# Optimization experiments

Hardware: AMD Instinct MI355X
Metric: run time of the kernel (lower is better)

## Reference

```python
import jax, jax.numpy as jnp
import numpy as np

D = 256  # model dim, used for 1/sqrt(d) scaling


def setup_inputs() -> dict:
    key = jax.random.key(0)
    ks = jax.random.split(key, 6)
    B, N, Dm, K = 4, 8192, 256, 256
    s = 0.02
    return {
        "I": jax.random.normal(ks[0], (B, N, Dm), dtype=jnp.float32),
        "Wq": jax.random.normal(ks[1], (Dm, Dm), dtype=jnp.float32) * s,
        "Wk": jax.random.normal(ks[2], (Dm, Dm), dtype=jnp.float32) * s,
        "Wv": jax.random.normal(ks[3], (Dm, Dm), dtype=jnp.float32) * s,
        "We": jax.random.normal(ks[4], (K, N), dtype=jnp.float32) * s,
        "Wf": jax.random.normal(ks[5], (K, N), dtype=jnp.float32) * s,
    }


def reference(I, Wq, Wk, Wv, We, Wf):
    # I: [B, n, d]; nn.Linear applies x @ W.T
    Q = jnp.einsum("bnd,ed->bne", I, Wq)          # [B, n, d]
    K = jnp.einsum("bnd,ed->bne", I, Wk)          # [B, n, d]
    V = jnp.einsum("bnd,ed->bne", I, Wv)          # [B, n, d]
    # E projects K along the sequence axis: K^T [B,d,n] -> [B,d,k]
    Ke = jnp.einsum("bnd,kn->bdk", K, We)         # [B, d, k]
    # F projects V along the sequence axis, then transpose back: [B,k,d]
    Vf = jnp.einsum("bnd,kn->bkd", V, Wf)         # [B, k, d]
    scale = 1.0 / jnp.sqrt(jnp.asarray(D, dtype=Q.dtype))
    PBar = jnp.einsum("bnd,bdk->bnk", Q, Ke) * scale  # [B, n, k]
    PBar = jax.nn.softmax(PBar, axis=2)
    # dropout omitted (eval / deterministic reference)
    Head = jnp.einsum("bnk,bkd->bnd", PBar, Vf)   # [B, n, d]
    return Head
```

## Files before the change

kernel.cpp:

```cpp
#include <hip/hip_runtime.h>
#include <stdint.h>


typedef unsigned short u16;
typedef __attribute__((ext_vector_type(8))) __bf16 bf16x8;
typedef __attribute__((ext_vector_type(4))) float f32x4;
typedef __attribute__((ext_vector_type(4))) unsigned short u16x4;
typedef __attribute__((ext_vector_type(8))) unsigned short u16x8;

__device__ __forceinline__ u16 f2bf(float f) {
  unsigned int u = __float_as_uint(f);
  u += 0x7FFFu + ((u >> 16) & 1u);
  return (u16)(u >> 16);
}

__device__ __forceinline__ void gld_lds16(const void* g, void* l) {
  __builtin_amdgcn_global_load_lds((const __attribute__((address_space(1))) void*)g,
                                   (__attribute__((address_space(3))) void*)l, 16, 0, 0);
}

__device__ __forceinline__ void stage_tile(const u16* src, long long ld, long long kb,
                                           u16* lds, int tid) {
#pragma unroll
  for (int r = 0; r < 4; ++r) {
    const int off = r * 4096 + tid * 16;
    const int row = off >> 7;
    const int colb = (off & 127) ^ ((row & 7) << 4);
    gld_lds16(src + (long long)row * ld + kb + (colb >> 1), (char*)lds + off);
  }
}

__device__ __forceinline__ void mfma_step(const u16* Alds, const u16* Blds, int lane, int wr,
                                          int wc, f32x4 (&acc)[4][4]) {
#pragma unroll
  for (int kk = 0; kk < 2; ++kk) {
    const int ko2 = (kk * 32 + (lane >> 4) * 8) * 2;
    bf16x8 a[4], b[4];
#pragma unroll
    for (int m = 0; m < 4; ++m) {
      const int ar = wr + m * 16 + (lane & 15);
      a[m] = *(const bf16x8*)((const char*)Alds + ((ar * 128 + ko2) ^ ((ar & 7) << 4)));
    }
#pragma unroll
    for (int n = 0; n < 4; ++n) {
      const int br = wc + n * 16 + (lane & 15);
      b[n] = *(const bf16x8*)((const char*)Blds + ((br * 128 + ko2) ^ ((br & 7) << 4)));
    }
#pragma unroll
    for (int m = 0; m < 4; ++m)
#pragma unroll
      for (int n = 0; n < 4; ++n)
        acc[m][n] = __builtin_amdgcn_mfma_f32_16x16x32_bf16(a[m], b[n], acc[m][n], 0, 0, 0);
  }
}

__global__ __launch_bounds__(256) void k0(const float* __restrict__ I,
                                          const float* __restrict__ Wq,
                                          const float* __restrict__ Wk,
                                          const float* __restrict__ Wv,
                                          const float* __restrict__ We,
                                          const float* __restrict__ Wf,
                                          u16* __restrict__ Ibf, u16* __restrict__ IT,
                                          u16* __restrict__ WqT, u16* __restrict__ WkT,
                                          u16* __restrict__ WvB, u16* __restrict__ WeB,
                                          u16* __restrict__ WfB) {
  const int p = blockIdx.x, t = threadIdx.x;
  if (p < 2080) {
    __shared__ u16 T[4096];
    const float* src;
    u16 *dT, *dS;
    long long srow, scol, tld;
    if (p < 2048) {
      const int b = p >> 9, id = p & 511;
      src = I + (long long)b * 2097152;
      srow = (long long)(id >> 2) * 64;
      scol = (long long)(id & 3) * 64;
      dS = Ibf + (long long)b * 2097152;
      dT = IT + (long long)b * 2097152;
      tld = 8192;
    } else {
      const int q = p - 2048;
      src = (q < 16) ? Wq : Wk;
      const int id = q & 15;
      srow = (long long)(id >> 2) * 64;
      scol = (long long)(id & 3) * 64;
      dS = nullptr;
      dT = (q < 16) ? WqT : WkT;
      tld = 256;
    }
    const int cc = t & 15, rL = t >> 4;
#pragma unroll
    for (int i = 0; i < 4; ++i) {
      const int r = rL + 16 * i;
      f32x4 v = *(const f32x4*)(src + (srow + r) * 256 + scol + cc * 4);
      u16x4 o = {f2bf(v[0]), f2bf(v[1]), f2bf(v[2]), f2bf(v[3])};
      if (dS) *(u16x4*)(dS + (srow + r) * 256 + scol + cc * 4) = o;
      const int P = (cc + (r & 15) + 4 * (r >> 4)) & 15;
      *(u16x4*)&T[r * 64 + P * 4] = o;
    }
    __syncthreads();
    const int dd = t >> 2, ch2 = t & 3;
    u16 buf[16];
#pragma unroll
    for (int j = 0; j < 16; ++j) {
      const int P = ((dd >> 2) + j + 4 * ch2) & 15;
      buf[j] = T[(ch2 * 16 + j) * 64 + P * 4 + (dd & 3)];
    }
    u16* dp = dT + (scol + dd) * tld + srow + ch2 * 16;
    *(u16x8*)dp = *(u16x8*)&buf[0];
    *(u16x8*)(dp + 8) = *(u16x8*)&buf[8];
  } else {
    const long long base = (long long)(p - 2080) * 4096;
#pragma unroll
    for (int rnd = 0; rnd < 4; ++rnd) {
      const long long e = base + rnd * 1024 + t * 4;
      const float* s;
      u16* d;
      long long eo;
      if (e < 65536) { s = Wv; d = WvB; eo = e; }
      else if (e < 2162688) { s = We; d = WeB; eo = e - 65536; }
      else { s = Wf; d = WfB; eo = e - 2162688; }
      f32x4 v = *(const f32x4*)(s + eo);
      *(u16x4*)(d + eo) = u16x4{f2bf(v[0]), f2bf(v[1]), f2bf(v[2]), f2bf(v[3])};
    }
  }
}

__global__ __launch_bounds__(256) void k1(const u16* __restrict__ WqT,
                                          const u16* __restrict__ WkT,
                                          const u16* __restrict__ WeB,
                                          const u16* __restrict__ WfB,
                                          const u16* __restrict__ IT,
                                          float* __restrict__ Pp, u16* __restrict__ G) {
  __shared__ u16 Alds[8192];
  __shared__ u16 Blds[8192];
  const int tid = threadIdx.x, lane = tid & 63, w = tid >> 6;
  const int wr = (w >> 1) * 64, wc = (w & 1) * 64;
  const u16 *A, *Bp;
  long long lda, k0, crow, ccol;
  int nkt;
  float* Cf = nullptr;
  u16* Cb = nullptr;
  if (blockIdx.x >= 512) {
    const int tl = blockIdx.x - 512;
    crow = (long long)(tl >> 1) * 128;
    ccol = (long long)(tl & 1) * 128;
    A = WqT + crow * 256;
    Bp = WkT + ccol * 256;
    lda = 256; k0 = 0; nkt = 4;
    Cb = G;
  } else {
    const int l = ((blockIdx.x & 7) << 6) + (blockIdx.x >> 3);
    const int mT = l & 1, nT = (l >> 1) & 1, s = (l >> 2) & 15, b = (l >> 6) & 3, op = l >> 8;
    A = (op ? WfB : WeB) + (long long)mT * 128 * 8192;
    Bp = IT + (long long)b * 2097152 + (long long)nT * 128 * 8192;
    lda = 8192;
    k0 = (long long)s * 512;
    nkt = 8;
    Cf = Pp + ((long long)(op * 4 + b) * 16 + s) * 65536;
    crow = (long long)mT * 128;
    ccol = (long long)nT * 128;
  }

  f32x4 acc[4][4];
#pragma unroll
  for (int m = 0; m < 4; ++m)
#pragma unroll
    for (int n = 0; n < 4; ++n) acc[m][n] = f32x4{0.f, 0.f, 0.f, 0.f};

  for (int kt = 0; kt < nkt; ++kt) {
    __syncthreads();
    stage_tile(A, lda, k0 + kt * 64, Alds, tid);
    stage_tile(Bp, lda, k0 + kt * 64, Blds, tid);
    __syncthreads();
    mfma_step(Alds, Blds, lane, wr, wc, acc);
  }

  const int r0 = (lane >> 4) * 4, c0 = lane & 15;
#pragma unroll
  for (int m = 0; m < 4; ++m)
#pragma unroll
    for (int n = 0; n < 4; ++n) {
      const long long row = crow + wr + m * 16 + r0;
      const long long col = ccol + wc + n * 16 + c0;
#pragma unroll
      for (int j = 0; j < 4; ++j) {
        if (Cf) Cf[(row + j) * 256 + col] = acc[m][n][j];
        else Cb[(row + j) * 256 + col] = f2bf(acc[m][n][j]);
      }
    }
}

__global__ __launch_bounds__(256) void reduce16(const float* __restrict__ P,
                                                u16* __restrict__ O) {
  const long long t = (long long)blockIdx.x * 256 + threadIdx.x;
  const long long g = t >> 14;
  const long long e = (t & 16383) << 2;
  const float* p = P + g * 1048576 + e;
  f32x4 s = {0.f, 0.f, 0.f, 0.f};
#pragma unroll
  for (int i = 0; i < 16; ++i) s += *(const f32x4*)(p + i * 65536);
  u16x4 o = {f2bf(s[0]), f2bf(s[1]), f2bf(s[2]), f2bf(s[3])};
  *(u16x4*)(O + g * 65536 + e) = o;
}

__global__ __launch_bounds__(256) void k3(const u16* __restrict__ SS, const u16* __restrict__ G,
                                          const u16* __restrict__ WvB, u16* __restrict__ Me,
                                          u16* __restrict__ VfT) {
  __shared__ u16 Alds[8192];
  __shared__ u16 Blds[8192];
  const int tid = threadIdx.x, lane = tid & 63, w = tid >> 6;
  const int wr = (w >> 1) * 64, wc = (w & 1) * 64;
  const int u = blockIdx.x;
  const int path = u >> 4, b = (u >> 2) & 3, mT = (u >> 1) & 1, nT = u & 1;
  const u16 *A, *Bp;
  u16* C;
  if (path == 0) { A = SS + b * 65536; Bp = G; C = Me + b * 65536; }
  else { A = WvB; Bp = SS + (4 + b) * 65536; C = VfT + b * 65536; }
  A += (long long)mT * 128 * 256;
  Bp += (long long)nT * 128 * 256;

  f32x4 acc[4][4];
#pragma unroll
  for (int m = 0; m < 4; ++m)
#pragma unroll
    for (int n = 0; n < 4; ++n) acc[m][n] = f32x4{0.f, 0.f, 0.f, 0.f};

  for (int kt = 0; kt < 4; ++kt) {
    __syncthreads();
    stage_tile(A, 256, kt * 64, Alds, tid);
    stage_tile(Bp, 256, kt * 64, Blds, tid);
    __syncthreads();
    mfma_step(Alds, Blds, lane, wr, wc, acc);
  }

  const int r0 = (lane >> 4) * 4, c0 = lane & 15;
#pragma unroll
  for (int m = 0; m < 4; ++m)
#pragma unroll
    for (int n = 0; n < 4; ++n) {
      const int row = mT * 128 + wr + m * 16 + r0;
      const int col = nT * 128 + wc + n * 16 + c0;
#pragma unroll
      for (int j = 0; j < 4; ++j) C[(row + j) * 256 + col] = f2bf(acc[m][n][j]);
    }
}

__device__ __forceinline__ void stage_bs(const u16* src, u16* Bs, int tid) {
#pragma unroll
  for (int r = 0; r < 8; ++r) {
    const int off = r * 4096 + tid * 16;
    const int row = off >> 7;
    const int colb = (off & 127) ^ ((row & 7) << 4);
    gld_lds16(src + row * 256 + (colb >> 1), (char*)Bs + off);
  }
}

__global__ __launch_bounds__(256) void flash3(const u16* __restrict__ Q,
                                              const u16* __restrict__ KeT,
                                              const u16* __restrict__ VfT,
                                              float* __restrict__ out) {
  __shared__ u16 Qs[16384];
  __shared__ u16 Bs[16384];
  __shared__ float Ms[256];
  __shared__ float Ss[256];
  const int tid = threadIdx.x;
  const int lane = tid & 63;
  const int w = tid >> 6;
  const int wc = w * 64;
  const int l = ((blockIdx.x & 7) << 6) + (blockIdx.x >> 3);
  const long long R0 = (long long)l * 64;
  const int batch = (int)(R0 >> 13);
  const u16* KeTb = KeT + (long long)batch * 65536;
  const u16* VfTb = VfT + (long long)batch * 65536;
  const int r0 = (lane >> 4) * 4, c0 = lane & 15;

#pragma unroll
  for (int r = 0; r < 8; ++r) {
    const int off = r * 4096 + tid * 16;
    const int row = off >> 9;
    const int colb = (off & 511) ^ ((row & 7) << 4);
    gld_lds16(Q + (R0 + row) * 256 + (colb >> 1), (char*)Qs + off);
  }

  f32x4 acc[4][4];
#pragma unroll
  for (int m = 0; m < 4; ++m)
#pragma unroll
    for (int n = 0; n < 4; ++n) acc[m][n] = f32x4{0.f, 0.f, 0.f, 0.f};

  for (int kc = 0; kc < 4; ++kc) {
    __syncthreads();
    stage_bs(KeTb + kc * 64, Bs, tid);
    __syncthreads();
#pragma unroll
    for (int kk = 0; kk < 2; ++kk) {
      const int ko = kk * 32 + (lane >> 4) * 8;
      bf16x8 a[4], b[4];
#pragma unroll
      for (int m = 0; m < 4; ++m) {
        const int ar = m * 16 + (lane & 15);
        a[m] = *(const bf16x8*)((const char*)Qs +
                                ((ar * 512 + (kc * 64 + ko) * 2) ^ ((ar & 7) << 4)));
      }
#pragma unroll
      for (int n = 0; n < 4; ++n) {
        const int br = wc + n * 16 + (lane & 15);
        b[n] = *(const bf16x8*)((const char*)Bs + ((br * 128 + ko * 2) ^ ((br & 7) << 4)));
      }
#pragma unroll
      for (int m = 0; m < 4; ++m)
#pragma unroll
        for (int n = 0; n < 4; ++n)
          acc[m][n] = __builtin_amdgcn_mfma_f32_16x16x32_bf16(a[m], b[n], acc[m][n], 0, 0, 0);
    }
  }

  float red[4][4];
#pragma unroll
  for (int m = 0; m < 4; ++m)
#pragma unroll
    for (int j = 0; j < 4; ++j)
      red[m][j] = fmaxf(fmaxf(acc[m][0][j], acc[m][1][j]), fmaxf(acc[m][2][j], acc[m][3][j]));
#pragma unroll
  for (int d = 1; d < 16; d <<= 1)
#pragma unroll
    for (int m = 0; m < 4; ++m)
#pragma unroll
      for (int j = 0; j < 4; ++j) red[m][j] = fmaxf(red[m][j], __shfl_xor(red[m][j], d));
  if ((lane & 15) == 0) {
#pragma unroll
    for (int m = 0; m < 4; ++m)
#pragma unroll
      for (int j = 0; j < 4; ++j) Ms[(m * 16 + r0 + j) * 4 + w] = red[m][j];
  }
  __syncthreads();
  float gm[4][4];
#pragma unroll
  for (int m = 0; m < 4; ++m)
#pragma unroll
    for (int j = 0; j < 4; ++j) {
      const f32x4 t = *(const f32x4*)&Ms[(m * 16 + r0 + j) * 4];
      gm[m][j] = fmaxf(fmaxf(t[0], t[1]), fmaxf(t[2], t[3]));
    }
#pragma unroll
  for (int m = 0; m < 4; ++m)
#pragma unroll
    for (int j = 0; j < 4; ++j) {
      float s = 0.f;
#pragma unroll
      for (int n = 0; n < 4; ++n) {
        const float e = __expf((acc[m][n][j] - gm[m][j]) * 0.0625f);
        acc[m][n][j] = e;
        s += e;
      }
      red[m][j] = s;
    }
#pragma unroll
  for (int d = 1; d < 16; d <<= 1)
#pragma unroll
    for (int m = 0; m < 4; ++m)
#pragma unroll
      for (int j = 0; j < 4; ++j) red[m][j] += __shfl_xor(red[m][j], d);
  if ((lane & 15) == 0) {
#pragma unroll
    for (int m = 0; m < 4; ++m)
#pragma unroll
      for (int j = 0; j < 4; ++j) Ss[(m * 16 + r0 + j) * 4 + w] = red[m][j];
  }
  __syncthreads();
#pragma unroll
  for (int m = 0; m < 4; ++m)
#pragma unroll
    for (int j = 0; j < 4; ++j) {
      const int row = m * 16 + r0 + j;
      const f32x4 t = *(const f32x4*)&Ss[row * 4];
      const float inv = 1.0f / (t[0] + t[1] + t[2] + t[3]);
#pragma unroll
      for (int n = 0; n < 4; ++n) {
        const int col = wc + n * 16 + c0;
        *(u16*)((char*)Qs + ((row * 512 + col * 2) ^ ((row & 7) << 4))) =
            f2bf(acc[m][n][j] * inv);
      }
    }
#pragma unroll
  for (int m = 0; m < 4; ++m)
#pragma unroll
    for (int n = 0; n < 4; ++n) acc[m][n] = f32x4{0.f, 0.f, 0.f, 0.f};

  for (int kc = 0; kc < 4; ++kc) {
    __syncthreads();
    stage_bs(VfTb + kc * 64, Bs, tid);
    __syncthreads();
#pragma unroll
    for (int kk = 0; kk < 2; ++kk) {
      const int ko = kk * 32 + (lane >> 4) * 8;
      bf16x8 a[4], b[4];
#pragma unroll
      for (int m = 0; m < 4; ++m) {
        const int ar = m * 16 + (lane & 15);
        a[m] = *(const bf16x8*)((const char*)Qs +
                                ((ar * 512 + (kc * 64 + ko) * 2) ^ ((ar & 7) << 4)));
      }
#pragma unroll
      for (int n = 0; n < 4; ++n) {
        const int br = wc + n * 16 + (lane & 15);
        b[n] = *(const bf16x8*)((const char*)Bs + ((br * 128 + ko * 2) ^ ((br & 7) << 4)));
      }
#pragma unroll
      for (int m = 0; m < 4; ++m)
#pragma unroll
        for (int n = 0; n < 4; ++n)
          acc[m][n] = __builtin_amdgcn_mfma_f32_16x16x32_bf16(a[m], b[n], acc[m][n], 0, 0, 0);
    }
  }

#pragma unroll
  for (int m = 0; m < 4; ++m)
#pragma unroll
    for (int n = 0; n < 4; ++n) {
      const long long row = R0 + m * 16 + r0;
      const int col = wc + n * 16 + c0;
#pragma unroll
      for (int j = 0; j < 4; ++j) out[(row + j) * 256 + col] = acc[m][n][j];
    }
}

extern "C" void kernel_launch(void* const* d_in, const int* in_sizes, int n_in, void* d_out,
                              int out_size, void* d_ws, size_t ws_size, hipStream_t stream) {
  (void)in_sizes; (void)n_in; (void)out_size; (void)ws_size;
  const float* I  = (const float*)d_in[0];
  const float* Wq = (const float*)d_in[1];
  const float* Wk = (const float*)d_in[2];
  const float* Wv = (const float*)d_in[3];
  const float* We = (const float*)d_in[4];
  const float* Wf = (const float*)d_in[5];
  float* out = (float*)d_out;
  char* ws = (char*)d_ws;

  u16* Ibf  = (u16*)(ws + 0);
  u16* IT   = (u16*)(ws + 16777216);
  u16* WqT  = (u16*)(ws + 33554432);
  u16* WkT  = (u16*)(ws + 33685504);
  u16* WvB  = (u16*)(ws + 33816576);
  u16* WeB  = (u16*)(ws + 33947648);
  u16* WfB  = (u16*)(ws + 38141952);
  u16* G    = (u16*)(ws + 42336256);
  float* Pp = (float*)(ws + 42467328);
  u16* SS   = (u16*)(ws + 76021760);
  u16* Me   = (u16*)(ws + 77070336);
  u16* VfT  = (u16*)(ws + 77594624);

  k0<<<3120, 256, 0, stream>>>(I, Wq, Wk, Wv, We, Wf, Ibf, IT, WqT, WkT, WvB, WeB, WfB);
  k1<<<516, 256, 0, stream>>>(WqT, WkT, WeB, WfB, IT, Pp, G);
  reduce16<<<512, 256, 0, stream>>>(Pp, SS);
  k3<<<32, 256, 0, stream>>>(SS, G, WvB, Me, VfT);
  flash3<<<512, 256, 0, stream>>>(Ibf, Me, VfT, out);
}
```

Baseline: 171.0 us.

## Double-buffer LDS tiles in k1 and k3 to overlap loads with MFMA

Result: no change. 173.2 us (+1.3%).

```diff
diff --git a/kernel.cpp b/kernel.cpp
--- a/kernel.cpp
+++ b/kernel.cpp
@@ -9,9 +9,9 @@
 typedef __attribute__((ext_vector_type(8))) unsigned short u16x8;
 
 __device__ __forceinline__ u16 f2bf(float f) {
-  unsigned int u = __float_as_uint(f);
-  u += 0x7FFFu + ((u >> 16) & 1u);
-  return (u16)(u >> 16);
+  union { __bf16 h; u16 u; } v;
+  v.h = (__bf16)f;
+  return v.u;
 }
 
 __device__ __forceinline__ void gld_lds16(const void* g, void* l) {
@@ -132,8 +132,8 @@
                                           const u16* __restrict__ WfB,
                                           const u16* __restrict__ IT,
                                           float* __restrict__ Pp, u16* __restrict__ G) {
-  __shared__ u16 Alds[8192];
-  __shared__ u16 Blds[8192];
+  __shared__ u16 Alds[2][8192];
+  __shared__ u16 Blds[2][8192];
   const int tid = threadIdx.x, lane = tid & 63, w = tid >> 6;
   const int wr = (w >> 1) * 64, wc = (w & 1) * 64;
   const u16 *A, *Bp;
@@ -168,12 +168,18 @@
 #pragma unroll
     for (int n = 0; n < 4; ++n) acc[m][n] = f32x4{0.f, 0.f, 0.f, 0.f};
 
+  stage_tile(A, lda, k0, Alds[0], tid);
+  stage_tile(Bp, lda, k0, Blds[0], tid);
+  __syncthreads();
+  int cur = 0;
   for (int kt = 0; kt < nkt; ++kt) {
-    __syncthreads();
-    stage_tile(A, lda, k0 + kt * 64, Alds, tid);
-    stage_tile(Bp, lda, k0 + kt * 64, Blds, tid);
-    __syncthreads();
-    mfma_step(Alds, Blds, lane, wr, wc, acc);
+    if (kt + 1 < nkt) {
+      stage_tile(A, lda, k0 + (kt + 1) * 64, Alds[cur ^ 1], tid);
+      stage_tile(Bp, lda, k0 + (kt + 1) * 64, Blds[cur ^ 1], tid);
+    }
+    mfma_step(Alds[cur], Blds[cur], lane, wr, wc, acc);
+    __syncthreads();
+    cur ^= 1;
   }
 
   const int r0 = (lane >> 4) * 4, c0 = lane & 15;
@@ -207,8 +213,8 @@
 __global__ __launch_bounds__(256) void k3(const u16* __restrict__ SS, const u16* __restrict__ G,
                                           const u16* __restrict__ WvB, u16* __restrict__ Me,
                                           u16* __restrict__ VfT) {
-  __shared__ u16 Alds[8192];
-  __shared__ u16 Blds[8192];
+  __shared__ u16 Alds[2][8192];
+  __shared__ u16 Blds[2][8192];
   const int tid = threadIdx.x, lane = tid & 63, w = tid >> 6;
   const int wr = (w >> 1) * 64, wc = (w & 1) * 64;
   const int u = blockIdx.x;
@@ -226,12 +232,18 @@
 #pragma unroll
     for (int n = 0; n < 4; ++n) acc[m][n] = f32x4{0.f, 0.f, 0.f, 0.f};
 
+  stage_tile(A, 256, 0, Alds[0], tid);
+  stage_tile(Bp, 256, 0, Blds[0], tid);
+  __syncthreads();
+  int cur = 0;
   for (int kt = 0; kt < 4; ++kt) {
-    __syncthreads();
-    stage_tile(A, 256, kt * 64, Alds, tid);
-    stage_tile(Bp, 256, kt * 64, Blds, tid);
-    __syncthreads();
-    mfma_step(Alds, Blds, lane, wr, wc, acc);
+    if (kt + 1 < 4) {
+      stage_tile(A, 256, (kt + 1) * 64, Alds[cur ^ 1], tid);
+      stage_tile(Bp, 256, (kt + 1) * 64, Blds[cur ^ 1], tid);
+    }
+    mfma_step(Alds[cur], Blds[cur], lane, wr, wc, acc);
+    __syncthreads();
+    cur ^= 1;
   }
 
   const int r0 = (lane >> 4) * 4, c0 = lane & 15;
```
